# Kernel tuning notes

Measured on AMD Instinct MI355X. Metric: run time of the kernel, lower is better.

The kernel has to match this reference:

```python
import jax, jax.numpy as jnp
import numpy as np

FS = 44100.0
TWO_PI = 2.0 * np.pi


def setup_inputs() -> dict:
    key = jax.random.key(0)
    ks = jax.random.split(key, 12)
    B, T, H, NF, NB = 4, 64000, 96, 4, 8
    f0 = jax.random.uniform(ks[0], (B, T, 1), minval=100.0, maxval=400.0)
    amplitudes = jax.random.uniform(ks[1], (B, T, H))
    vibrato_rate = 5.0 + jax.random.uniform(ks[2], (B, T, 1))
    vibrato_depth = 0.2 * jax.random.uniform(ks[3], (B, T, 1))
    ff = jnp.array([800.0, 1150.0, 2900.0, 3900.0], dtype=jnp.float32)
    fb = jnp.array([80.0, 90.0, 120.0, 130.0], dtype=jnp.float32)
    fg = jnp.array([1.0, 0.5, 0.25, 0.1], dtype=jnp.float32)
    formant_freqs = ff[None, None] * (0.9 + 0.2 * jax.random.uniform(ks[4], (B, T, NF)))
    formant_bandwidths = fb[None, None] * (0.9 + 0.2 * jax.random.uniform(ks[5], (B, T, NF)))
    formant_gains = fg[None, None] * (0.9 + 0.2 * jax.random.uniform(ks[6], (B, T, NF)))
    glottal_open_quotient = 0.5 + 0.4 * jax.random.uniform(ks[7], (B, T, 1))
    phase_coherence = jax.random.uniform(ks[8], (B, T, 1))
    breathiness = 0.3 * jax.random.uniform(ks[9], (B, T, 1))
    breath_spectral_shape = jax.random.uniform(ks[10], (B, T, NB))
    initial_phase = jnp.zeros((B, 1, 1), dtype=jnp.float32)
    return dict(f0=f0, amplitudes=amplitudes, vibrato_rate=vibrato_rate,
                vibrato_depth=vibrato_depth, formant_freqs=formant_freqs,
                formant_bandwidths=formant_bandwidths, formant_gains=formant_gains,
                glottal_open_quotient=glottal_open_quotient,
                phase_coherence=phase_coherence, breathiness=breathiness,
                breath_spectral_shape=breath_spectral_shape, initial_phase=initial_phase)


def _breath_noise(noise, spectral_weights):
    # noise: [B,T]; spectral_weights: [B,n_bands] (mid frame) -> normalized shaped noise [B,T]
    B, T = noise.shape
    n_bands = spectral_weights.shape[1]
    shaped = jnp.zeros_like(noise)
    for i in range(n_bands):  # small fixed band loop (structurally distinct kernel sizes)
        smooth = 2.0 ** (i / 2.0)
        ksz = max(3, int(128 / smooth))
        if ksz % 2 == 0:
            ksz += 1
        g = np.exp(-np.arange(-(ksz // 2), ksz // 2 + 1) ** 2 / (2.0 * (ksz / 6.0) ** 2))
        kern = jnp.asarray(g / g.sum(), dtype=jnp.float32)
        smoothed = jax.lax.conv_general_dilated(
            noise[:, None, :], kern[None, None, :], (1,), 'SAME')[:, 0, :]
        shaped = shaped + smoothed * spectral_weights[:, i:i + 1]
    mean = shaped.mean(axis=1, keepdims=True)
    std = shaped.std(axis=1, ddof=1, keepdims=True) + 1e-8
    return (shaped - mean) / std


def _forward(f0, amplitudes, vibrato_rate, vibrato_depth, formant_freqs,
             formant_bandwidths, formant_gains, glottal_open_quotient,
             phase_coherence, breathiness, breath_spectral_shape, initial_phase, noise):
    B, T, H = amplitudes.shape
    fs = FS
    # --- vibrato ---
    t = (jnp.arange(T, dtype=jnp.float32) / fs)[None, :, None]
    vib_factor = 2.0 ** (vibrato_depth / 12.0)
    vib_mult = jnp.exp(jnp.sin(TWO_PI * vibrato_rate * t) * jnp.log(vib_factor))
    f0_vib = jnp.where(f0 > 0, f0 * vib_mult, f0)  # B,T,1
    # --- per-harmonic phases via cumulative fundamental phase ---
    fund_phase = jnp.cumsum(TWO_PI * f0_vib / fs, axis=1) + initial_phase  # B,T,1
    n = jnp.arange(1, H + 1, dtype=jnp.float32)  # harmonic numbers
    phases = fund_phase * n  # B,T,H
    # --- phase coherence: blend higher harmonics toward n * fundamental ---
    coherent = fund_phase * n[1:]
    blended = phase_coherence * coherent + (1.0 - phase_coherence) * phases[:, :, 1:]
    phases = jnp.concatenate([phases[:, :, :1], blended], axis=2)
    # --- remove above Nyquist ---
    amp = jnp.where(f0_vib * n < fs / 2.0, amplitudes, jnp.zeros_like(amplitudes))
    # --- glottal flow model ---
    norm_phase = jnp.mod(phases, TWO_PI) / TWO_PI
    oq = glottal_open_quotient
    half_pi = jnp.float32(np.pi / 2.0)
    rising = jnp.sin(norm_phase / oq * half_pi) ** 2
    falling = jnp.cos((norm_phase - oq) / (1.0 - oq) * half_pi) ** 2
    flow = jnp.where(norm_phase < oq, rising, falling) - 0.5
    signal = jnp.sum(flow * amp, axis=-1)  # B,T
    # --- formant filter (mid-frame params, vectorized over batch & formants) ---
    mid = T // 2
    freqs = jnp.fft.rfftfreq(T, d=1.0 / fs).astype(jnp.float32)  # [F]
    fmid = formant_freqs[:, mid][:, :, None]       # B,NF,1
    bwmid = formant_bandwidths[:, mid][:, :, None]
    gmid = formant_gains[:, mid][:, :, None]
    resp = (gmid / (1.0 + ((freqs[None, None, :] - fmid) / (bwmid / 2.0)) ** 2)).sum(1)  # B,F
    filtered = jnp.fft.irfft(jnp.fft.rfft(signal) * resp, n=T)  # B,T
    # --- breath noise mix ---
    breath = _breath_noise(noise, breath_spectral_shape[:, mid])  # B,T
    br = breathiness[:, :, 0]
    out = filtered * (1.0 - br) + breath * br
    final_phase = jnp.mod(fund_phase[:, -1:, :], TWO_PI)  # B,1,1
    return out, final_phase


def reference(f0, amplitudes, vibrato_rate, vibrato_depth, formant_freqs,
              formant_bandwidths, formant_gains, glottal_open_quotient,
              phase_coherence, breathiness, breath_spectral_shape, initial_phase):
    B, T = f0.shape[0], f0.shape[1]
    noise = jax.random.normal(jax.random.key(42), (B, T), dtype=jnp.float32)
    return _forward(f0, amplitudes, vibrato_rate, vibrato_depth, formant_freqs,
                    formant_bandwidths, formant_gains, glottal_open_quotient,
                    phase_coherence, breathiness, breath_spectral_shape,
                    initial_phase, noise)
```

## Files before the change

kernel.cpp:

```cpp
#include <hip/hip_runtime.h>
#include <math.h>
#include <stdint.h>

#define B_ 4
#define T_ 64000
#define H_ 96
#define NCH 1000
#define TT_ 64
#define TWO_PI_D 6.283185307179586

typedef float2 cplx;
__device__ __forceinline__ cplx cadd(cplx a, cplx b){ return make_float2(a.x+b.x, a.y+b.y); }
__device__ __forceinline__ cplx csub(cplx a, cplx b){ return make_float2(a.x-b.x, a.y-b.y); }
__device__ __forceinline__ cplx cmul(cplx a, cplx b){ return make_float2(a.x*b.x - a.y*b.y, a.x*b.y + a.y*b.x); }

__device__ float  g_dpf[B_*T_];
__device__ unsigned char g_hcnt[B_*T_];
__device__ float  g_signal[B_*T_];
__device__ float  g_shaped[B_*T_];
__device__ float2 g_W1[2*512*125];
__device__ float2 g_Z[2*125*512];
__device__ double g_chunksum[B_*NCH];
__device__ double g_stats[B_*2];
__device__ double g_part[B_*250*2];

__device__ __forceinline__ double fsin64(double x){
  double z = x * 0.63661977236758138243;
  double fn = floor(z + 0.5);
  int k = (int)fn;
  const double p1 = 1.57079632673412561417e+00;
  const double p2 = 6.07710050650619224932e-11;
  double r = x - fn*p1;
  r = r - fn*p2;
  double s = r*r;
  double ps = 1.58969099521155010221e-10;
  ps = ps*s - 2.50507602534068634195e-08;
  ps = ps*s + 2.75573137070700676789e-06;
  ps = ps*s - 1.98412698298579493134e-04;
  ps = ps*s + 8.33333333332248946124e-03;
  ps = ps*s - 1.66666666666666324348e-01;
  double sr = r + r*s*ps;
  double pc = -1.13596475577881948265e-11;
  pc = pc*s + 2.08757232129817482790e-09;
  pc = pc*s - 2.75573143513906633035e-07;
  pc = pc*s + 2.48015872894767294178e-05;
  pc = pc*s - 1.38888888888741095749e-03;
  pc = pc*s + 4.16666666666666019037e-02;
  double cr = 1.0 - 0.5*s + s*s*pc;
  int m = k & 3;
  return (m==0) ? sr : (m==1) ? cr : (m==2) ? -sr : -cr;
}

__device__ __forceinline__ double fexp_small(double x){
  double p = 1.9841269841269841e-04;
  p = p*x + 1.3888888888888889e-03;
  p = p*x + 8.3333333333333332e-03;
  p = p*x + 4.1666666666666664e-02;
  p = p*x + 1.6666666666666666e-01;
  p = p*x + 0.5;
  p = p*x + 1.0;
  p = p*x + 1.0;
  return p;
}

__device__ __forceinline__ uint32_t rotl32(uint32_t x, int r){ return (x<<r)|(x>>(32-r)); }

__device__ __forceinline__ uint32_t threefry_bits(uint32_t i){
  uint32_t x0 = 0u, x1 = i;
  const uint32_t ks0 = 0u, ks1 = 42u, ks2 = 0u ^ 42u ^ 0x1BD11BDAu;
  x0 += ks0; x1 += ks1;
  #define TFR(r) { x0 += x1; x1 = rotl32(x1, r); x1 ^= x0; }
  TFR(13) TFR(15) TFR(26) TFR(6)   x0 += ks1; x1 += ks2 + 1u;
  TFR(17) TFR(29) TFR(16) TFR(24)  x0 += ks2; x1 += ks0 + 2u;
  TFR(13) TFR(15) TFR(26) TFR(6)   x0 += ks0; x1 += ks1 + 3u;
  TFR(17) TFR(29) TFR(16) TFR(24)  x0 += ks1; x1 += ks2 + 4u;
  TFR(13) TFR(15) TFR(26) TFR(6)   x0 += ks2; x1 += ks0 + 5u;
  #undef TFR
  return x0 ^ x1;
}

__device__ __forceinline__ float bits_to_normal(uint32_t bits){
  uint32_t mbits = (bits >> 9) | 0x3F800000u;
  float f = __uint_as_float(mbits) - 1.0f;
  const float lo = -0.99999994f;
  float x = f * 2.0f + lo;
  x = fmaxf(lo, x);
  float w = -log1pf(-x*x);
  float p;
  if (w < 5.0f){
    w -= 2.5f;
    p = 2.81022636e-08f;
    p = fmaf(p, w, 3.43273939e-07f);
    p = fmaf(p, w, -3.5233877e-06f);
    p = fmaf(p, w, -4.39150654e-06f);
    p = fmaf(p, w, 0.00021858087f);
    p = fmaf(p, w, -0.00125372503f);
    p = fmaf(p, w, -0.00417768164f);
    p = fmaf(p, w, 0.246640727f);
    p = fmaf(p, w, 1.50140941f);
  } else {
    w = sqrtf(w) - 3.0f;
    p = -0.000200214257f;
    p = fmaf(p, w, 0.000100950558f);
    p = fmaf(p, w, 0.00134934322f);
    p = fmaf(p, w, -0.00367342844f);
    p = fmaf(p, w, 0.00573950773f);
    p = fmaf(p, w, -0.0076224613f);
    p = fmaf(p, w, 0.00943887047f);
    p = fmaf(p, w, 1.00167406f);
    p = fmaf(p, w, 2.83297682f);
  }
  return 1.4142135623730951f * (p * x);
}

__constant__ int KSZc[8] = {129,91,65,45,33,23,17,11};

__global__ __launch_bounds__(256) void k_prep(const float* __restrict__ bss,
                                              const float* __restrict__ f0,
                                              const float* __restrict__ vr,
                                              const float* __restrict__ vd){
  int b = blockIdx.x / 250, c = blockIdx.x % 250;
  int t0 = c*256, tid = threadIdx.x;
  __shared__ __align__(16) float ns4[4][388];
  __shared__ __align__(16) float kl[132];
  __shared__ float wn[8];
  {
    int i = tid >> 5, l32 = tid & 31;
    int ksz = KSZc[i];
    float sig = (float)ksz / 6.0f;
    float inv2s2 = 1.0f/(2.0f*sig*sig);
    int ctr = ksz>>1;
    float s = 0.f;
    for (int j = l32; j < ksz; j += 32){
      float d = (float)(j - ctr);
      s += expf(-d*d*inv2s2);
    }
    #pragma unroll
    for (int o=1;o<32;o<<=1) s += __shfl_xor(s, o);
    if (l32 == 0) wn[i] = bss[((size_t)b*T_ + T_/2)*8 + i] / s;
  }
  for (int j = tid; j < 384; j += 256){
    int t = t0 - 64 + j;
    float v = 0.f;
    if (t >= 0 && t < T_) v = bits_to_normal(threefry_bits((uint32_t)(b*T_ + t)));
    ns4[0][j] = v;
  }
  __syncthreads();
  if (tid < 129){
    int tau = tid - 64;
    float acc = 0.f;
    #pragma unroll
    for (int i=0;i<8;i++){
      int ksz = KSZc[i]; int hw = ksz>>1;
      if (tau >= -hw && tau <= hw){
        float sig = (float)ksz/6.0f;
        float inv2s2 = 1.0f/(2.0f*sig*sig);
        acc += expf(-(float)(tau*tau)*inv2s2) * wn[i];
      }
    }
    kl[tid] = acc;
  }
  for (int k = tid; k < 381; k += 256){
    float v1 = ns4[0][k+1];
    float v2 = ns4[0][k+2];
    float v3 = ns4[0][k+3];
    ns4[1][k] = v1; ns4[2][k] = v2; ns4[3][k] = v3;
  }
  __syncthreads();
  int al = tid & 3, bk = tid & ~3;
  const float4* nsA = (const float4*)&ns4[al][bk];
  const float4* kl4 = (const float4*)kl;
  float A0=0.f, A1=0.f, A2=0.f, A3=0.f;
  #pragma unroll
  for (int j4=0;j4<32;j4++){
    float4 nv = nsA[j4];
    float4 kv = kl4[j4];
    A0 = fmaf(nv.x, kv.x, A0);
    A1 = fmaf(nv.y, kv.y, A1);
    A2 = fmaf(nv.z, kv.z, A2);
    A3 = fmaf(nv.w, kv.w, A3);
  }
  float acc = (A0+A1)+(A2+A3);
  acc = fmaf(ns4[0][tid+128], kl[128], acc);
  g_shaped[b*T_ + t0 + tid] = acc;
  double xx = (double)acc;
  double s1 = xx, s2 = xx*xx;
  for (int o=1;o<64;o<<=1){ s1 += __shfl_down(s1,o); s2 += __shfl_down(s2,o); }
  __shared__ double pa1[4], pa2[4];
  int lane = tid&63, wid = tid>>6;
  if (lane==0){ pa1[wid]=s1; pa2[wid]=s2; }
  __syncthreads();
  if (tid==0){
    g_part[(b*250+c)*2]   = pa1[0]+pa1[1]+pa1[2]+pa1[3];
    g_part[(b*250+c)*2+1] = pa2[0]+pa2[1]+pa2[2]+pa2[3];
  }
  int t = t0 + tid;
  int idx = b*T_ + t;
  double tt = (double)t * 2.2675736961451248e-05;
  double argd = TWO_PI_D * (double)vr[idx] * tt;
  double argr = argd - TWO_PI_D * floor(argd * 0.15915494309189535);
  float svf = __sinf((float)argr);
  double lm = (double)vd[idx] * 0.057762265046662105;
  double vm = fexp_small((double)svf * lm);
  double f0s = (double)f0[idx];
  double f0v = (f0s > 0.0) ? f0s * vm : f0s;
  int cnt;
  if (f0v <= 0.0) cnt = 96;
  else {
    int n = (int)(22050.0f / (float)f0v);
    if (!((double)n * f0v < 22050.0)) n--;
    if ((double)(n+1) * f0v < 22050.0) n++;
    double dlo = 22050.0 - (double)n * f0v;
    double dhi = (double)(n+1) * f0v - 22050.0;
    if (dlo < 0.01 || dhi < 0.01){
      double sv_d = fsin64(argd);
      double vm_d = fexp_small(sv_d * lm);
      double f0x = f0s * vm_d;
      int n2 = (int)(22050.0f / (float)f0x);
      if (!((double)n2 * f0x < 22050.0)) n2--;
      if ((double)(n2+1) * f0x < 22050.0) n2++;
      n = n2;
      f0v = f0x;
    }
    cnt = (n < 0) ? 0 : ((n > 96) ? 96 : n);
  }
  g_hcnt[idx] = (unsigned char)cnt;
  double v = f0v * 1.4247585730565955e-04;
  g_dpf[idx] = (float)v;
  for (int o=1;o<64;o<<=1) v += __shfl_down(v, o);
  if (lane == 0) g_chunksum[b*NCH + c*4 + wid] = v;
}

__global__ __launch_bounds__(256) void k_signal(const float* __restrict__ amps,
                                                const float* __restrict__ goq,
                                                const float* __restrict__ iph,
                                                float* __restrict__ out_final){
  __shared__ float ph[TT_];
  int b = blockIdx.x / NCH, c = blockIdx.x % NCH;
  int t0 = c*TT_;
  int tid = threadIdx.x;
  if (tid < 64){
    double s = 0.0;
    for (int ch = tid; ch < c; ch += 64) s += g_chunksum[b*NCH + ch];
    for (int o=1;o<64;o<<=1) s += __shfl_xor(s, o);
    double base = s + (double)iph[b];
    int idx = b*T_ + t0 + tid;
    double v = (double)g_dpf[idx];
    for (int o=1;o<64;o<<=1){ double u = __shfl_up(v, o); if (tid >= o) v += u; }
    ph[tid] = (float)fmod(base + v, TWO_PI_D);
    if (c == NCH-1 && tid == 63) out_final[b] = (float)fmod(base + v, TWO_PI_D);
  }
  __syncthreads();
  int tl = tid >> 2, part = tid & 3;
  int idx = b*T_ + t0 + tl;
  float r = ph[tl];
  int hc = (int)g_hcnt[idx];
  float oq = goq[idx];
  float k1 = 3.14159265358979f / oq;
  float k2 = 3.14159265358979f / (1.0f - oq);
  float offA = 3.14159265358979f;
  float offB = -oq * k2;
  float r0 = r * 0.15915494309189535f;
  int hbase = part*24;
  float fr = (float)(hbase+1) * r0;
  fr = fr - floorf(fr);
  float sum = 0.f;
  const float4* Ar = (const float4*)(amps + ((size_t)b*T_ + t0 + tl)*H_ + part*24);
  #pragma unroll
  for (int j4=0;j4<6;j4++){
    int h0 = hbase + j4*4;
    if (h0 >= hc) break;
    float4 a4 = Ar[j4];
    float av0[4] = {a4.x, a4.y, a4.z, a4.w};
    #pragma unroll
    for (int e=0;e<4;e++){
      int h = h0 + e;
      float amp = (h < hc) ? av0[e] : 0.0f;
      bool ris = fr < oq;
      float kk  = ris ? k1 : k2;
      float off = ris ? offA : offB;
      float cv = __cosf(fmaf(fr, kk, off));
      sum = fmaf(cv, amp, sum);
      fr += r0;
      fr = fr - floorf(fr);
    }
  }
  sum += __shfl_xor(sum, 1);
  sum += __shfl_xor(sum, 2);
  if (part == 0) g_signal[idx] = 0.5f * sum;
}

template<int SGN>
__device__ __forceinline__ float2* fft512_r4(float2* bufA, float2* bufB, int tid){
  float2* src = bufA; float2* dst = bufB;
  #pragma unroll
  for (int st=0; st<4; st++){
    const int s = 1<<(2*st);
    const int n = 512>>(2*st);
    const int m = n>>2;
    if (tid < 128){
      int p = tid / s;
      int q = tid - p*s;
      float2 a0 = src[q + s*p];
      float2 a1 = src[q + s*(p+m)];
      float2 a2 = src[q + s*(p+2*m)];
      float2 a3 = src[q + s*(p+3*m)];
      float2 t0 = cadd(a0,a2), t1 = csub(a0,a2);
      float2 t2 = cadd(a1,a3), t3 = csub(a1,a3);
      float2 it3 = make_float2(-(float)SGN*t3.y, (float)SGN*t3.x);
      float2 r0 = cadd(t0,t2);
      float2 r1 = cadd(t1,it3);
      float2 r2 = csub(t0,t2);
      float2 r3 = csub(t1,it3);
      float ba = (float)SGN * ((float)(2.0*M_PI)/(float)n) * (float)p;
      dst[q + s*(4*p+0)] = r0;
      float sw,cw;
      __sincosf(ba, &sw, &cw);
      dst[q + s*(4*p+1)] = cmul(make_float2(cw,sw), r1);
      __sincosf(2.f*ba, &sw, &cw);
      dst[q + s*(4*p+2)] = cmul(make_float2(cw,sw), r2);
      __sincosf(3.f*ba, &sw, &cw);
      dst[q + s*(4*p+3)] = cmul(make_float2(cw,sw), r3);
    }
    __syncthreads();
    float2* tp = src; src = dst; dst = tp;
  }
  {
    float2 a = src[tid];
    float2 bb = src[tid+256];
    dst[tid]     = cadd(a,bb);
    dst[tid+256] = csub(a,bb);
    __syncthreads();
    float2* tp = src; src = dst; dst = tp;
  }
  return src;
}

__device__ __forceinline__ cplx w5k(int k, float sgn){
  const float C[5] = {1.f, 0.30901699f, -0.80901699f, -0.80901699f, 0.30901699f};
  const float S[5] = {0.f, 0.95105652f, 0.58778525f, -0.58778525f, -0.95105652f};
  return make_float2(C[k], sgn*S[k]);
}

template<int SGN>
__device__ __forceinline__ float2* fft125_rows(float2* bufA, float2* bufB, int tid){
  float2* src = bufA; float2* dst = bufB;
  #pragma unroll
  for (int st=0; st<3; st++){
    const int s = (st==0)?1:((st==1)?5:25);
    const int n = (st==0)?125:((st==1)?25:5);
    const int m = n/5;
    if (tid < 200){
      int row = tid/25, w = tid - row*25;
      int p = w/s, q = w - p*s;
      int base = row*125 + q;
      float2 a0 = src[base + s*p];
      float2 a1 = src[base + s*(p+m)];
      float2 a2 = src[base + s*(p+2*m)];
      float2 a3 = src[base + s*(p+3*m)];
      float2 a4 = src[base + s*(p+4*m)];
      #pragma unroll
      for (int r2=0;r2<5;r2++){
        float2 acc = a0;
        acc = cadd(acc, cmul(a1, w5k((1*r2)%5, (float)SGN)));
        acc = cadd(acc, cmul(a2, w5k((2*r2)%5, (float)SGN)));
        acc = cadd(acc, cmul(a3, w5k((3*r2)%5, (float)SGN)));
        acc = cadd(acc, cmul(a4, w5k((4*r2)%5, (float)SGN)));
        float ang = (float)SGN * ((float)(2.0*M_PI)/(float)n) * (float)(p*r2);
        float sw,cw; __sincosf(ang,&sw,&cw);
        dst[base + s*(5*p+r2)] = cmul(make_float2(cw,sw), acc);
      }
    }
    __syncthreads();
    float2* tp = src; src = dst; dst = tp;
  }
  return src;
}

__global__ __launch_bounds__(256) void k_fft512_fwd(){
  int p = blockIdx.x / 125, n1 = blockIdx.x % 125;
  int tid = threadIdx.x;
  __shared__ float2 bufA[512];
  __shared__ float2 bufB[512];
  const float* sa = g_signal + (size_t)(2*p)*T_;
  const float* sb = g_signal + (size_t)(2*p+1)*T_;
  for (int i=tid;i<512;i+=256) bufA[i] = make_float2(sa[n1 + 125*i], sb[n1 + 125*i]);
  __syncthreads();
  float2* res = fft512_r4<-1>(bufA, bufB, tid);
  for (int i=tid;i<512;i+=256){
    float ang = -(float)(2.0*M_PI/64000.0) * (float)(n1*i);
    float sw,cw; __sincosf(ang,&sw,&cw);
    g_W1[((size_t)p*512 + i)*125 + n1] = cmul(make_float2(cw,sw), res[i]);
  }
  if (blockIdx.x < B_){
    int b = blockIdx.x;
    double s1=0.0, s2=0.0;
    if (tid < 250){ s1 = g_part[(b*250+tid)*2]; s2 = g_part[(b*250+tid)*2+1]; }
    for (int o=1;o<64;o<<=1){ s1 += __shfl_down(s1,o); s2 += __shfl_down(s2,o); }
    __shared__ double a1[4], a2[4];
    int lane = tid&63, wid = tid>>6;
    if (lane==0){ a1[wid]=s1; a2[wid]=s2; }
    __syncthreads();
    if (tid==0){
      double S1=a1[0]+a1[1]+a1[2]+a1[3], S2=a2[0]+a2[1]+a2[2]+a2[3];
      double mean = S1 / (double)T_;
      double var = (S2 - (double)T_*mean*mean) / (double)(T_-1);
      if (var < 0.0) var = 0.0;
      double rstd = 1.0/(sqrt(var) + 1e-8);
      g_stats[b*2] = mean; g_stats[b*2+1] = rstd;
    }
  }
}

__global__ __launch_bounds__(256) void k_fft125_mid(const float* __restrict__ ffq,
                                                    const float* __restrict__ fbw,
                                                    const float* __restrict__ fgn){
  int p = blockIdx.x / 64;
  int j = blockIdx.x % 64;
  int tid = threadIdx.x;
  __shared__ float2 bufA[1000];
  __shared__ float2 bufB[1000];
  int k2r[8];
  #pragma unroll
  for (int l=0;l<8;l++){
    int k2;
    if (l < 4) k2 = 4*j + l;
    else if (j==0 && l==4) k2 = 256;
    else k2 = 512 - 4*j - (l-4);
    k2r[l] = k2;
  }
  for (int i=tid;i<1000;i+=256){
    int l = i/125, n1 = i - l*125;
    bufA[i] = g_W1[((size_t)p*512 + k2r[l])*125 + n1];
  }
  float fca[4], bwa[4], ga[4], fcb[4], bwb[4], gb[4];
  int ba = 2*p, bb = 2*p+1;
  #pragma unroll
  for (int q=0;q<4;q++){
    size_t ia = ((size_t)ba*T_ + T_/2)*4 + q;
    size_t ib = ((size_t)bb*T_ + T_/2)*4 + q;
    fca[q]=ffq[ia]; bwa[q]=fbw[ia]; ga[q]=fgn[ia];
    fcb[q]=ffq[ib]; bwb[q]=fbw[ib]; gb[q]=fgn[ib];
  }
  __syncthreads();
  float2* X = fft125_rows<-1>(bufA, bufB, tid);
  float2* Y = (X == bufA) ? bufB : bufA;
  for (int i=tid;i<1000;i+=256){
    int l = i/125, k1 = i - l*125;
    int k2 = k2r[l];
    int lm = ((j==0) && (l==0 || l==4)) ? l : (l^4);
    int k1m = (k2 == 0) ? ((k1==0)?0:(125-k1)) : (124-k1);
    float2 Z1 = X[l*125 + k1];
    float2 Z2 = X[lm*125 + k1m];
    float xax = 0.5f*(Z1.x + Z2.x), xay = 0.5f*(Z1.y - Z2.y);
    float xbx = 0.5f*(Z1.y + Z2.y), xby = -0.5f*(Z1.x - Z2.x);
    int f = k2 + 512*k1;
    int fi = (f <= 32000) ? f : (64000 - f);
    float freq = (float)fi * 0.6890625f;
    float ra = 0.f, rb = 0.f;
    #pragma unroll
    for (int q=0;q<4;q++){
      float da = (freq - fca[q]) / (bwa[q]*0.5f);
      ra += ga[q] / (1.0f + da*da);
      float db = (freq - fcb[q]) / (bwb[q]*0.5f);
      rb += gb[q] / (1.0f + db*db);
    }
    float yax = ra*xax, yay = ra*xay;
    float ybx = rb*xbx, yby = rb*xby;
    Y[i] = make_float2(yax - yby, yay + ybx);
  }
  __syncthreads();
  float2* res2 = fft125_rows<1>(Y, X, tid);
  for (int i=tid;i<1000;i+=256){
    int l = i/125, n1 = i - l*125;
    int k2 = k2r[l];
    float ang = (float)(2.0*M_PI/64000.0) * (float)(n1*k2);
    float sw,cw; __sincosf(ang,&sw,&cw);
    g_Z[((size_t)p*125 + n1)*512 + k2] = cmul(make_float2(cw,sw), res2[i]);
  }
}

__global__ __launch_bounds__(256) void k_fft512_inv(const float* __restrict__ brth,
                                                    float* __restrict__ outp){
  int p = blockIdx.x / 125, n1 = blockIdx.x % 125;
  int tid = threadIdx.x;
  __shared__ float2 bufA[512];
  __shared__ float2 bufB[512];
  const float2* gin = g_Z + ((size_t)p*125 + n1)*512;
  for (int i=tid;i<512;i+=256) bufA[i] = gin[i];
  __syncthreads();
  float2* res = fft512_r4<1>(bufA, bufB, tid);
  int ba = 2*p, bb = 2*p+1;
  float mean_a = (float)g_stats[ba*2], rstd_a = (float)g_stats[ba*2+1];
  float mean_b = (float)g_stats[bb*2], rstd_b = (float)g_stats[bb*2+1];
  for (int i=tid;i<512;i+=256){
    int t = n1 + 125*i;
    float2 v = res[i];
    {
      int idx = ba*T_ + t;
      float filt = v.x * (1.0f/64000.0f);
      float br = brth[idx];
      float breath = (g_shaped[idx] - mean_a) * rstd_a;
      outp[idx] = filt*(1.0f - br) + breath*br;
    }
    {
      int idx = bb*T_ + t;
      float filt = v.y * (1.0f/64000.0f);
      float br = brth[idx];
      float breath = (g_shaped[idx] - mean_b) * rstd_b;
      outp[idx] = filt*(1.0f - br) + breath*br;
    }
  }
}

extern "C" void kernel_launch(void* const* d_in, const int* in_sizes, int n_in,
                              void* d_out, int out_size, void* d_ws, size_t ws_size,
                              hipStream_t stream){
  (void)in_sizes; (void)n_in; (void)out_size; (void)d_ws; (void)ws_size;
  const float* f0   = (const float*)d_in[0];
  const float* amps = (const float*)d_in[1];
  const float* vr   = (const float*)d_in[2];
  const float* vd   = (const float*)d_in[3];
  const float* ffq  = (const float*)d_in[4];
  const float* fbw  = (const float*)d_in[5];
  const float* fgn  = (const float*)d_in[6];
  const float* goq  = (const float*)d_in[7];
  const float* brth = (const float*)d_in[9];
  const float* bss  = (const float*)d_in[10];
  const float* iph  = (const float*)d_in[11];
  float* out = (float*)d_out;
  float* out_final = out + (size_t)B_*T_;

  k_prep<<<B_*250,256,0,stream>>>(bss, f0, vr, vd);
  k_signal<<<B_*NCH,256,0,stream>>>(amps, goq, iph, out_final);
  k_fft512_fwd<<<250,256,0,stream>>>();
  k_fft125_mid<<<128,256,0,stream>>>(ffq, fbw, fgn);
  k_fft512_inv<<<250,256,0,stream>>>(brth, out);
}
```

Measured before the change: 63.80 us.

## Move breath-noise convolution from prep kernel into the signal synthesis kernel

```diff
diff --git a/kernel.cpp b/kernel.cpp
--- a/kernel.cpp
+++ b/kernel.cpp
@@ -18,11 +18,12 @@
 __device__ unsigned char g_hcnt[B_*T_];
 __device__ float  g_signal[B_*T_];
 __device__ float  g_shaped[B_*T_];
+__device__ float  g_Kcomb[B_][132];
 __device__ float2 g_W1[2*512*125];
 __device__ float2 g_Z[2*125*512];
 __device__ double g_chunksum[B_*NCH];
 __device__ double g_stats[B_*2];
-__device__ double g_part[B_*250*2];
+__device__ double g_part[B_*NCH*2];
 
 __device__ __forceinline__ double fsin64(double x){
   double z = x * 0.63661977236758138243;
@@ -115,84 +116,44 @@
 
 __constant__ int KSZc[8] = {129,91,65,45,33,23,17,11};
 
-__global__ __launch_bounds__(256) void k_prep(const float* __restrict__ bss,
-                                              const float* __restrict__ f0,
-                                              const float* __restrict__ vr,
-                                              const float* __restrict__ vd){
+__global__ __launch_bounds__(256) void k_phase(const float* __restrict__ bss,
+                                               const float* __restrict__ f0,
+                                               const float* __restrict__ vr,
+                                               const float* __restrict__ vd){
   int b = blockIdx.x / 250, c = blockIdx.x % 250;
   int t0 = c*256, tid = threadIdx.x;
-  __shared__ __align__(16) float ns4[4][388];
-  __shared__ __align__(16) float kl[132];
-  __shared__ float wn[8];
-  {
-    int i = tid >> 5, l32 = tid & 31;
-    int ksz = KSZc[i];
-    float sig = (float)ksz / 6.0f;
-    float inv2s2 = 1.0f/(2.0f*sig*sig);
-    int ctr = ksz>>1;
-    float s = 0.f;
-    for (int j = l32; j < ksz; j += 32){
-      float d = (float)(j - ctr);
-      s += expf(-d*d*inv2s2);
-    }
-    #pragma unroll
-    for (int o=1;o<32;o<<=1) s += __shfl_xor(s, o);
-    if (l32 == 0) wn[i] = bss[((size_t)b*T_ + T_/2)*8 + i] / s;
-  }
-  for (int j = tid; j < 384; j += 256){
-    int t = t0 - 64 + j;
-    float v = 0.f;
-    if (t >= 0 && t < T_) v = bits_to_normal(threefry_bits((uint32_t)(b*T_ + t)));
-    ns4[0][j] = v;
-  }
-  __syncthreads();
-  if (tid < 129){
-    int tau = tid - 64;
-    float acc = 0.f;
-    #pragma unroll
-    for (int i=0;i<8;i++){
-      int ksz = KSZc[i]; int hw = ksz>>1;
-      if (tau >= -hw && tau <= hw){
-        float sig = (float)ksz/6.0f;
-        float inv2s2 = 1.0f/(2.0f*sig*sig);
-        acc += expf(-(float)(tau*tau)*inv2s2) * wn[i];
+  if (c == 0){
+    __shared__ float wn[8];
+    {
+      int i = tid >> 5, l32 = tid & 31;
+      int ksz = KSZc[i];
+      float sig = (float)ksz / 6.0f;
+      float inv2s2 = 1.0f/(2.0f*sig*sig);
+      int ctr = ksz>>1;
+      float s = 0.f;
+      for (int j = l32; j < ksz; j += 32){
+        float d = (float)(j - ctr);
+        s += expf(-d*d*inv2s2);
       }
-    }
-    kl[tid] = acc;
-  }
-  for (int k = tid; k < 381; k += 256){
-    float v1 = ns4[0][k+1];
-    float v2 = ns4[0][k+2];
-    float v3 = ns4[0][k+3];
-    ns4[1][k] = v1; ns4[2][k] = v2; ns4[3][k] = v3;
-  }
-  __syncthreads();
-  int al = tid & 3, bk = tid & ~3;
-  const float4* nsA = (const float4*)&ns4[al][bk];
-  const float4* kl4 = (const float4*)kl;
-  float A0=0.f, A1=0.f, A2=0.f, A3=0.f;
-  #pragma unroll
-  for (int j4=0;j4<32;j4++){
-    float4 nv = nsA[j4];
-    float4 kv = kl4[j4];
-    A0 = fmaf(nv.x, kv.x, A0);
-    A1 = fmaf(nv.y, kv.y, A1);
-    A2 = fmaf(nv.z, kv.z, A2);
-    A3 = fmaf(nv.w, kv.w, A3);
-  }
-  float acc = (A0+A1)+(A2+A3);
-  acc = fmaf(ns4[0][tid+128], kl[128], acc);
-  g_shaped[b*T_ + t0 + tid] = acc;
-  double xx = (double)acc;
-  double s1 = xx, s2 = xx*xx;
-  for (int o=1;o<64;o<<=1){ s1 += __shfl_down(s1,o); s2 += __shfl_down(s2,o); }
-  __shared__ double pa1[4], pa2[4];
-  int lane = tid&63, wid = tid>>6;
-  if (lane==0){ pa1[wid]=s1; pa2[wid]=s2; }
-  __syncthreads();
-  if (tid==0){
-    g_part[(b*250+c)*2]   = pa1[0]+pa1[1]+pa1[2]+pa1[3];
-    g_part[(b*250+c)*2+1] = pa2[0]+pa2[1]+pa2[2]+pa2[3];
+      #pragma unroll
+      for (int o=1;o<32;o<<=1) s += __shfl_xor(s, o);
+      if (l32 == 0) wn[i] = bss[((size_t)b*T_ + T_/2)*8 + i] / s;
+    }
+    __syncthreads();
+    if (tid < 129){
+      int tau = tid - 64;
+      float acc = 0.f;
+      #pragma unroll
+      for (int i=0;i<8;i++){
+        int ksz = KSZc[i]; int hw = ksz>>1;
+        if (tau >= -hw && tau <= hw){
+          float sig = (float)ksz/6.0f;
+          float inv2s2 = 1.0f/(2.0f*sig*sig);
+          acc += expf(-(float)(tau*tau)*inv2s2) * wn[i];
+        }
+      }
+      g_Kcomb[b][tid] = acc;
+    }
   }
   int t = t0 + tid;
   int idx = b*T_ + t;
@@ -227,15 +188,19 @@
   g_hcnt[idx] = (unsigned char)cnt;
   double v = f0v * 1.4247585730565955e-04;
   g_dpf[idx] = (float)v;
+  int lane = tid & 63, wid = tid >> 6;
   for (int o=1;o<64;o<<=1) v += __shfl_down(v, o);
   if (lane == 0) g_chunksum[b*NCH + c*4 + wid] = v;
 }
 
-__global__ __launch_bounds__(256) void k_signal(const float* __restrict__ amps,
-                                                const float* __restrict__ goq,
-                                                const float* __restrict__ iph,
-                                                float* __restrict__ out_final){
+__global__ __launch_bounds__(256) void k_sigbreath(const float* __restrict__ amps,
+                                                   const float* __restrict__ goq,
+                                                   const float* __restrict__ iph,
+                                                   float* __restrict__ out_final){
   __shared__ float ph[TT_];
+  __shared__ float ns[192];
+  __shared__ float kl[132];
+  __shared__ float shb[TT_];
   int b = blockIdx.x / NCH, c = blockIdx.x % NCH;
   int t0 = c*TT_;
   int tid = threadIdx.x;
@@ -250,8 +215,25 @@
     ph[tid] = (float)fmod(base + v, TWO_PI_D);
     if (c == NCH-1 && tid == 63) out_final[b] = (float)fmod(base + v, TWO_PI_D);
   }
+  {
+    int k = (tid < 64) ? tid + 128 : tid - 64;
+    int t = t0 - 64 + k;
+    float nv = 0.f;
+    if (t >= 0 && t < T_) nv = bits_to_normal(threefry_bits((uint32_t)(b*T_ + t)));
+    if (k < 192) ns[k] = nv;
+  }
+  if (tid >= 192){
+    for (int k = tid - 192; k < 129; k += 64) kl[k] = g_Kcomb[b][k];
+  }
   __syncthreads();
   int tl = tid >> 2, part = tid & 3;
+  {
+    float accb = 0.f;
+    for (int j = part; j < 129; j += 4) accb = fmaf(ns[tl + j], kl[j], accb);
+    accb += __shfl_xor(accb, 1);
+    accb += __shfl_xor(accb, 2);
+    if (part == 0) shb[tl] = accb;
+  }
   int idx = b*T_ + t0 + tl;
   float r = ph[tl];
   int hc = (int)g_hcnt[idx];
@@ -288,6 +270,18 @@
   sum += __shfl_xor(sum, 1);
   sum += __shfl_xor(sum, 2);
   if (part == 0) g_signal[idx] = 0.5f * sum;
+  __syncthreads();
+  if (tid < 64){
+    float sv = shb[tid];
+    g_shaped[b*T_ + t0 + tid] = sv;
+    double xx = (double)sv;
+    double s1 = xx, s2 = xx*xx;
+    for (int o=1;o<64;o<<=1){ s1 += __shfl_down(s1,o); s2 += __shfl_down(s2,o); }
+    if (tid == 0){
+      g_part[(b*NCH+c)*2]   = s1;
+      g_part[(b*NCH+c)*2+1] = s2;
+    }
+  }
 }
 
 template<int SGN>
@@ -395,7 +389,14 @@
   if (blockIdx.x < B_){
     int b = blockIdx.x;
     double s1=0.0, s2=0.0;
-    if (tid < 250){ s1 = g_part[(b*250+tid)*2]; s2 = g_part[(b*250+tid)*2+1]; }
+    if (tid < 250){
+      #pragma unroll
+      for (int k=0;k<4;k++){
+        int ch = tid*4 + k;
+        s1 += g_part[(b*NCH+ch)*2];
+        s2 += g_part[(b*NCH+ch)*2+1];
+      }
+    }
     for (int o=1;o<64;o<<=1){ s1 += __shfl_down(s1,o); s2 += __shfl_down(s2,o); }
     __shared__ double a1[4], a2[4];
     int lane = tid&63, wid = tid>>6;
@@ -531,8 +532,8 @@
   float* out = (float*)d_out;
   float* out_final = out + (size_t)B_*T_;
 
-  k_prep<<<B_*250,256,0,stream>>>(bss, f0, vr, vd);
-  k_signal<<<B_*NCH,256,0,stream>>>(amps, goq, iph, out_final);
+  k_phase<<<B_*250,256,0,stream>>>(bss, f0, vr, vd);
+  k_sigbreath<<<B_*NCH,256,0,stream>>>(amps, goq, iph, out_final);
   k_fft512_fwd<<<250,256,0,stream>>>();
   k_fft125_mid<<<128,256,0,stream>>>(ffq, fbw, fgn);
   k_fft512_inv<<<250,256,0,stream>>>(brth, out);
```

Measured after the change: 61.55 us. 1.04x faster.
